# Optimization experiments

Hardware: AMD Instinct MI355X
Metric: run time of the kernel (lower is better)

The kernel has to match this reference:

```python
import jax, jax.numpy as jnp
import numpy as np
import math

BS, SEQ, HID = 1, 2048, 2048
NH, NKV, HD = 32, 8, 64
BASE = 10000.0


def rotate_half(x):
    x1, x2 = x[..., : x.shape[-1] // 2], x[..., x.shape[-1] // 2 :]
    return jnp.concatenate((-x2, x1), axis=-1)


def setup_inputs() -> dict:
    key = jax.random.key(0)
    ks = jax.random.split(key, 6)
    s = 0.02
    return {
        "x": jax.random.normal(ks[0], (BS, SEQ, HID), dtype=jnp.float32),
        "attention_mask": jnp.zeros((BS, SEQ), dtype=jnp.float32),
        "position_ids": jnp.broadcast_to(jnp.arange(SEQ, dtype=jnp.int64 if jax.config.jax_enable_x64 else jnp.int32), (BS, SEQ)),
        "wq": jax.random.normal(ks[1], (HID, NH * HD), dtype=jnp.float32) * s,
        "wk": jax.random.normal(ks[2], (HID, NKV * HD), dtype=jnp.float32) * s,
        "wv": jax.random.normal(ks[3], (HID, NKV * HD), dtype=jnp.float32) * s,
        "wo": jax.random.normal(ks[4], (NH * HD, HID), dtype=jnp.float32) * s,
    }


def reference(x, attention_mask, position_ids, wq, wk, wv, wo):
    bs, seq, _ = x.shape
    groups = NH // NKV

    q = (x @ wq).reshape(bs, seq, NH, HD).transpose(0, 2, 1, 3)   # [b,H,S,D]
    k = (x @ wk).reshape(bs, seq, NKV, HD).transpose(0, 2, 1, 3)  # [b,Hkv,S,D]
    v = (x @ wv).reshape(bs, seq, NKV, HD).transpose(0, 2, 1, 3)

    # rotary embedding
    inv_freq = 1.0 / (BASE ** (jnp.arange(0, HD, 2, dtype=jnp.float32) / HD))  # [D/2]
    freqs = position_ids.astype(jnp.float32)[:, :, None] * inv_freq[None, None, :]  # [b,S,D/2]
    emb = jnp.concatenate((freqs, freqs), axis=-1)               # [b,S,D]
    cos = jnp.cos(emb)[:, None, :, :].astype(x.dtype)            # [b,1,S,D]
    sin = jnp.sin(emb)[:, None, :, :].astype(x.dtype)
    q = q * cos + rotate_half(q) * sin
    k = k * cos + rotate_half(k) * sin

    # repeat_kv (GQA expand)
    k = jnp.repeat(k, groups, axis=1)  # [b,H,S,D]
    v = jnp.repeat(v, groups, axis=1)

    scores = jnp.einsum("bhqd,bhkd->bhqk", q, k) / math.sqrt(HD)
    scores = scores + attention_mask[:, None, None, :]
    attn = jax.nn.softmax(scores.astype(jnp.float32), axis=-1).astype(q.dtype)
    out = jnp.einsum("bhqk,bhkd->bhqd", attn, v)                 # [b,H,S,D]
    out = out.transpose(0, 2, 1, 3).reshape(bs, seq, NH * HD)
    return out @ wo
```

## Files before the change

kernel.cpp:

```cpp
#include <hip/hip_runtime.h>

#define SEQ 2048
#define HID 2048
#define NH  32
#define NKV 8
#define HD  64

typedef _Float16 f16;
typedef __attribute__((ext_vector_type(4))) _Float16 f16x4;
typedef __attribute__((ext_vector_type(8))) _Float16 f16x8;
typedef __attribute__((ext_vector_type(2))) __fp16   h16x2;
typedef __attribute__((ext_vector_type(4))) float    f32x4;

__device__ __forceinline__ f32x4 mfma_16x16x32(f16x8 a, f16x8 b, f32x4 c) {
    return __builtin_amdgcn_mfma_f32_16x16x32_f16(a, b, c, 0, 0, 0);
}

__device__ __forceinline__ void async16(const void* g, void* l) {
    __builtin_amdgcn_global_load_lds(
        (const __attribute__((address_space(1))) void*)g,
        (__attribute__((address_space(3))) void*)l,
        16, 0, 0);
}

__global__ void prep_all(const float* __restrict__ x,
                         const float* __restrict__ wq, const float* __restrict__ wk,
                         const float* __restrict__ wv, const float* __restrict__ wo,
                         f16* __restrict__ xb,
                         f16* __restrict__ Wcat, f16* __restrict__ woT) {
    __shared__ float tile[32][33];
    int z = blockIdx.z;
    int tx = threadIdx.x, ty = threadIdx.y;
    if (z == 4) {
        int idx = (blockIdx.y * 64 + blockIdx.x) * 256 + ty * 32 + tx;
        int i = idx * 4;
        float4 v = *(const float4*)(x + i);
        f16x4 o = { (f16)v.x, (f16)v.y, (f16)v.z, (f16)v.w };
        *(f16x4*)(xb + i) = o;
        return;
    }
    const float* src; f16* dst; int C;
    if      (z == 0) { src = wq; dst = Wcat;                         C = 2048; }
    else if (z == 1) { src = wk; dst = Wcat + (size_t)2048 * 2048;   C = 512;  }
    else if (z == 2) { src = wv; dst = Wcat + (size_t)2560 * 2048;   C = 512;  }
    else             { src = wo; dst = woT;                          C = 2048; }
    int c0 = blockIdx.x * 32, r0 = blockIdx.y * 32;
    if (c0 >= C) return;
#pragma unroll
    for (int i = 0; i < 32; i += 8)
        tile[ty + i][tx] = src[(size_t)(r0 + ty + i) * C + c0 + tx];
    __syncthreads();
#pragma unroll
    for (int i = 0; i < 32; i += 8)
        dst[(size_t)(c0 + ty + i) * 2048 + r0 + tx] = (f16)tile[tx][ty + i];
}

template <int MODE>
__global__ __launch_bounds__(256)
void gemm_bt(const f16* __restrict__ A, const f16* __restrict__ BT,
             float* __restrict__ Cf, f16* __restrict__ Q, f16* __restrict__ Kk,
             f16* __restrict__ VT, const int* __restrict__ pos,
             const float* __restrict__ mask, int N, int K) {
    __shared__ f16 As[2][64 * 64];
    __shared__ f16 Bs[2][128 * 64];
    int t = threadIdx.x;
    int w = t >> 6, lane = t & 63, quad = lane >> 4, l15 = lane & 15;
    int wm = w >> 1, wn = w & 1;
    int m0 = blockIdx.y * 64, n0 = blockIdx.x * 128;
    int sw = l15 & 7;

    int r8 = lane >> 3;
    int cc = (lane & 7) ^ r8;
    const f16* Ag0 = A  + (size_t)(m0 + w * 16 + r8) * K + cc * 8;
    const f16* Ag1 = Ag0 + (size_t)8 * K;
    const f16* Bg  = BT + (size_t)(n0 + w * 32 + r8) * K + cc * 8;

    f32x4 acc[2][4] = {};

    async16(Ag0, &As[0][w * 1024]);
    async16(Ag1, &As[0][w * 1024 + 512]);
#pragma unroll
    for (int g = 0; g < 4; g++)
        async16(Bg + (size_t)(8 * g) * K, &Bs[0][w * 2048 + g * 512]);
    __syncthreads();

    int b = 0;
    for (int kt = 64; kt <= K; kt += 64) {
        if (kt < K) {
            async16(Ag0 + kt, &As[b ^ 1][w * 1024]);
            async16(Ag1 + kt, &As[b ^ 1][w * 1024 + 512]);
#pragma unroll
            for (int g = 0; g < 4; g++)
                async16(Bg + (size_t)(8 * g) * K + kt, &Bs[b ^ 1][w * 2048 + g * 512]);
        }
        f16x8 af[2][2], bf[4][2];
#pragma unroll
        for (int mi = 0; mi < 2; mi++) {
            int row = wm * 32 + mi * 16 + l15;
#pragma unroll
            for (int kh = 0; kh < 2; kh++)
                af[mi][kh] = *(const f16x8*)(&As[b][row * 64 + ((kh * 4 + quad) ^ sw) * 8]);
        }
#pragma unroll
        for (int ni = 0; ni < 4; ni++) {
            int row = wn * 64 + ni * 16 + l15;
#pragma unroll
            for (int kh = 0; kh < 2; kh++)
                bf[ni][kh] = *(const f16x8*)(&Bs[b][row * 64 + ((kh * 4 + quad) ^ sw) * 8]);
        }
#pragma unroll
        for (int mi = 0; mi < 2; mi++)
#pragma unroll
            for (int ni = 0; ni < 4; ni++) {
                acc[mi][ni] = mfma_16x16x32(af[mi][0], bf[ni][0], acc[mi][ni]);
                acc[mi][ni] = mfma_16x16x32(af[mi][1], bf[ni][1], acc[mi][ni]);
            }
        __syncthreads();
        b ^= 1;
    }

    int rb  = m0 + wm * 32 + quad * 4;
    int cbh = n0 + wn * 64;
    if (MODE == 0) {
        if (cbh < (NH + NKV) * HD) {
            bool isQ = cbh < NH * HD;
            f16* dst = isQ ? (Q  + (size_t)(cbh >> 6) * SEQ * HD)
                           : (Kk + (size_t)((cbh - NH * HD) >> 6) * SEQ * HD);
            float scale = isQ ? 0.18033688011112042f : 1.0f;
            float fr[2];
#pragma unroll
            for (int ni = 0; ni < 2; ni++)
                fr[ni] = __builtin_amdgcn_exp2f(
                    (float)(ni * 16 + l15) * -0.41524101186092029f);
#pragma unroll
            for (int mi = 0; mi < 2; mi++)
#pragma unroll
                for (int r = 0; r < 4; r++) {
                    int row = rb + mi * 16 + r;
                    float pv = (float)pos[row];
#pragma unroll
                    for (int ni = 0; ni < 2; ni++) {
                        float sn, cs;
                        __sincosf(pv * fr[ni], &sn, &cs);
                        float x1 = acc[mi][ni][r], x2 = acc[mi][ni + 2][r];
                        int d = ni * 16 + l15;
                        dst[(size_t)row * HD + d]      = (f16)(scale * (x1 * cs - x2 * sn));
                        dst[(size_t)row * HD + d + 32] = (f16)(scale * (x2 * cs + x1 * sn));
                    }
                }
        } else {
            const float LOG2E = 1.4426950408889634f;
#pragma unroll
            for (int mi = 0; mi < 2; mi++) {
                float4 mv = *(const float4*)(mask + rb + mi * 16);
                float em[4];
#pragma unroll
                for (int r = 0; r < 4; r++)
                    em[r] = __builtin_amdgcn_exp2f((&mv.x)[r] * LOG2E);
#pragma unroll
                for (int ni = 0; ni < 4; ni++) {
                    int c2 = cbh - (NH + NKV) * HD + ni * 16 + l15;
                    f16x4 v4;
                    ((h16x2*)&v4)[0] = __builtin_amdgcn_cvt_pkrtz(
                        acc[mi][ni][0] * em[0], acc[mi][ni][1] * em[1]);
                    ((h16x2*)&v4)[1] = __builtin_amdgcn_cvt_pkrtz(
                        acc[mi][ni][2] * em[2], acc[mi][ni][3] * em[3]);
                    *(f16x4*)(VT + (size_t)c2 * SEQ + rb + mi * 16) = v4;
                }
            }
        }
    } else {
#pragma unroll
        for (int mi = 0; mi < 2; mi++)
#pragma unroll
            for (int ni = 0; ni < 4; ni++)
#pragma unroll
                for (int r = 0; r < 4; r++)
                    Cf[(size_t)(rb + mi * 16 + r) * N + cbh + ni * 16 + l15] =
                        acc[mi][ni][r];
    }
}

__global__ __launch_bounds__(512)
void attn_fused(const f16* __restrict__ Qb, const f16* __restrict__ Kb,
                const f16* __restrict__ VTb, const float* __restrict__ mask,
                f16* __restrict__ Opart, float* __restrict__ Lpart) {
    __shared__ f16 Ks[2][64 * 64];
    __shared__ f16 Vs[2][64 * 64];
    __shared__ f16 Em[SEQ / 2];

    int t = threadIdx.x, w = t >> 6, lane = t & 63, quad = lane >> 4, l15 = lane & 15;
    int h = blockIdx.y, kvh = h >> 2, split = blockIdx.z;
    int qbase = blockIdx.x * 256 + w * 32;
    int key0  = split * (SEQ / 2);
    const f16* Qh = Qb  + (size_t)h   * SEQ * HD;
    const f16* Kh = Kb  + (size_t)kvh * SEQ * HD;
    const f16* Vh = VTb + (size_t)kvh * HD * SEQ;
    int sw = l15 & 7;
    const float LOG2E = 1.4426950408889634f;

    if (t < 128) {
        int idx = t * 8;
        float4 ma = *(const float4*)(mask + key0 + idx);
        float4 mb = *(const float4*)(mask + key0 + idx + 4);
        f16x8 e;
        ((h16x2*)&e)[0] = __builtin_amdgcn_cvt_pkrtz(
            __builtin_amdgcn_exp2f(ma.x * LOG2E), __builtin_amdgcn_exp2f(ma.y * LOG2E));
        ((h16x2*)&e)[1] = __builtin_amdgcn_cvt_pkrtz(
            __builtin_amdgcn_exp2f(ma.z * LOG2E), __builtin_amdgcn_exp2f(ma.w * LOG2E));
        ((h16x2*)&e)[2] = __builtin_amdgcn_cvt_pkrtz(
            __builtin_amdgcn_exp2f(mb.x * LOG2E), __builtin_amdgcn_exp2f(mb.y * LOG2E));
        ((h16x2*)&e)[3] = __builtin_amdgcn_cvt_pkrtz(
            __builtin_amdgcn_exp2f(mb.z * LOG2E), __builtin_amdgcn_exp2f(mb.w * LOG2E));
        *(f16x8*)(&Em[idx]) = e;
    }

    int r8 = lane >> 3;
    int cc = (lane & 7) ^ r8;
    bool isK = w < 4;
    int ws = isK ? w : (w - 4);
    const f16* g0;
    long gstep;
    if (isK) {
        int gk = 32 * (ws >> 1) + 4 * (ws & 1) + 8 * (r8 >> 2) + (r8 & 3);
        g0 = Kh + (size_t)(key0 + gk) * HD + cc * 8;
        gstep = (long)16 * HD;
    } else {
        g0 = Vh + (size_t)(ws * 16 + r8) * SEQ + key0 + cc * 8;
        gstep = (long)8 * SEQ;
    }
    const f16* g1 = g0 + gstep;
    long adv = isK ? (long)64 * HD : 64;
    int lr0 = ws * 16 * 64, lr1 = lr0 + 8 * 64;

    {
        f16* dst = isK ? &Ks[0][0] : &Vs[0][0];
        async16(g0, dst + lr0);
        async16(g1, dst + lr1);
    }

    f16x8 bq[2][2];
#pragma unroll
    for (int qg = 0; qg < 2; qg++)
#pragma unroll
        for (int ks = 0; ks < 2; ks++)
            bq[qg][ks] = *(const f16x8*)(Qh + (size_t)(qbase + qg * 16 + l15) * HD
                                            + ks * 32 + quad * 8);

    f32x4 o[4][2] = {};
    f32x4 ol[2]   = {};

    int c0 = (quad ^ sw) * 8, c1 = ((4 | quad) ^ sw) * 8;

    __syncthreads();
    int b = 0;

    for (int ktl = 0; ktl < SEQ / 128; ktl++) {
        if (ktl + 1 < SEQ / 128) {
            g0 += adv; g1 += adv;
            f16* dst = isK ? &Ks[b ^ 1][0] : &Vs[b ^ 1][0];
            async16(g0, dst + lr0);
            async16(g1, dst + lr1);
        }
        const f16* Kb_ = &Ks[b][0];
        const f16* Vb_ = &Vs[b][0];

        f32x4 st[4][2] = {};
#pragma unroll
        for (int ni = 0; ni < 4; ni++) {
            const f16* kr = Kb_ + (ni * 16 + l15) * 64;
            f16x8 ak0 = *(const f16x8*)(kr + c0);
            f16x8 ak1 = *(const f16x8*)(kr + c1);
#pragma unroll
            for (int qg = 0; qg < 2; qg++) {
                st[ni][qg] = mfma_16x16x32(ak0, bq[qg][0], st[ni][qg]);
                st[ni][qg] = mfma_16x16x32(ak1, bq[qg][1], st[ni][qg]);
            }
        }
        f16x8 pb[2][2];
#pragma unroll
        for (int ni = 0; ni < 4; ni++)
#pragma unroll
            for (int qg = 0; qg < 2; qg++) {
                h16x2 lo = __builtin_amdgcn_cvt_pkrtz(
                    __builtin_amdgcn_exp2f(st[ni][qg][0]),
                    __builtin_amdgcn_exp2f(st[ni][qg][1]));
                h16x2 hi = __builtin_amdgcn_cvt_pkrtz(
                    __builtin_amdgcn_exp2f(st[ni][qg][2]),
                    __builtin_amdgcn_exp2f(st[ni][qg][3]));
                ((h16x2*)&pb[qg][ni >> 1])[(ni & 1) * 2]     = lo;
                ((h16x2*)&pb[qg][ni >> 1])[(ni & 1) * 2 + 1] = hi;
            }
        f16x8 em0 = *(const f16x8*)(&Em[ktl * 64 + quad * 8]);
        f16x8 em1 = *(const f16x8*)(&Em[ktl * 64 + 32 + quad * 8]);
#pragma unroll
        for (int qg = 0; qg < 2; qg++) {
            ol[qg] = mfma_16x16x32(em0, pb[qg][0], ol[qg]);
            ol[qg] = mfma_16x16x32(em1, pb[qg][1], ol[qg]);
        }
#pragma unroll
        for (int dt = 0; dt < 4; dt++) {
            const f16* vr = Vb_ + (dt * 16 + l15) * 64;
            f16x8 av0 = *(const f16x8*)(vr + c0);
            f16x8 av1 = *(const f16x8*)(vr + c1);
#pragma unroll
            for (int qg = 0; qg < 2; qg++) {
                o[dt][qg] = mfma_16x16x32(av0, pb[qg][0], o[dt][qg]);
                o[dt][qg] = mfma_16x16x32(av1, pb[qg][1], o[dt][qg]);
            }
        }
        __syncthreads();
        b ^= 1;
    }

    if (quad == 0) {
#pragma unroll
        for (int qg = 0; qg < 2; qg++)
            Lpart[((size_t)split * NH + h) * SEQ + qbase + qg * 16 + l15] =
                ol[qg][0];
    }
    f16* Op = Opart + ((size_t)split * NH + h) * SEQ * HD;
#pragma unroll
    for (int dt = 0; dt < 4; dt++)
#pragma unroll
        for (int qg = 0; qg < 2; qg++) {
            f16x4 v4;
            ((h16x2*)&v4)[0] = __builtin_amdgcn_cvt_pkrtz(o[dt][qg][0], o[dt][qg][1]);
            ((h16x2*)&v4)[1] = __builtin_amdgcn_cvt_pkrtz(o[dt][qg][2], o[dt][qg][3]);
            *(f16x4*)(Op + (size_t)(qbase + qg * 16 + l15) * HD
                         + dt * 16 + quad * 4) = v4;
        }
}

__global__ void attn_combine(const f16* __restrict__ O, const float* __restrict__ L,
                             f16* __restrict__ ctx) {
    int idx = blockIdx.x * 256 + threadIdx.x;
    int c4  = idx & 511;
    int row = idx >> 9;
    int col = c4 * 4;
    int h   = col >> 6;
    float l = L[(size_t)h * SEQ + row] + L[(size_t)(NH + h) * SEQ + row];
    const f16* o0 = O + ((size_t)h * SEQ + row) * HD + (col & 63);
    const f16* o1 = o0 + (size_t)NH * SEQ * HD;
    f16x4 a = *(const f16x4*)o0, b = *(const f16x4*)o1;
    float inv = 1.0f / l;
    f16x4 r;
#pragma unroll
    for (int j = 0; j < 4; j++)
        r[j] = (f16)(((float)a[j] + (float)b[j]) * inv);
    *(f16x4*)(ctx + (size_t)row * (NH * HD) + col) = r;
}

extern "C" void kernel_launch(void* const* d_in, const int* in_sizes, int n_in,
                              void* d_out, int out_size, void* d_ws, size_t ws_size,
                              hipStream_t stream) {
    const float* x    = (const float*)d_in[0];
    const float* mask = (const float*)d_in[1];
    const int*   pos  = (const int*)  d_in[2];
    const float* wq   = (const float*)d_in[3];
    const float* wk   = (const float*)d_in[4];
    const float* wv   = (const float*)d_in[5];
    const float* wo   = (const float*)d_in[6];
    float* out = (float*)d_out;

    char* ws = (char*)d_ws;
    f16*   xb    = (f16*)(ws);
    f16*   Wcat  = (f16*)(ws + ((size_t)8  << 20));
    f16*   woT   = (f16*)(ws + ((size_t)20 << 20));
    f16*   Qb    = (f16*)(ws + ((size_t)28 << 20));
    f16*   Kb    = (f16*)(ws + ((size_t)36 << 20));
    f16*   VTb   = (f16*)(ws + ((size_t)38 << 20));
    f16*   Opart = (f16*)(ws);
    float* Lpart = (float*)(ws + ((size_t)16 << 20));
    f16*   ctx   = (f16*)(ws + ((size_t)28 << 20));

    prep_all<<<dim3(64, 64, 5), dim3(32, 8), 0, stream>>>(
        x, wq, wk, wv, wo, xb, Wcat, woT);

    gemm_bt<0><<<dim3(3072 / 128, 2048 / 64), 256, 0, stream>>>(
        xb, Wcat, nullptr, Qb, Kb, VTb, pos, mask, 3072, 2048);

    attn_fused<<<dim3(SEQ / 256, NH, 2), 512, 0, stream>>>(
        Qb, Kb, VTb, mask, Opart, Lpart);
    attn_combine<<<SEQ * NH * HD / 4 / 256, 256, 0, stream>>>(Opart, Lpart, ctx);

    gemm_bt<1><<<dim3(2048 / 128, 2048 / 64), 256, 0, stream>>>(
        ctx, woT, out, nullptr, nullptr, nullptr, nullptr, nullptr, 2048, 2048);
}
```

Measured before the change: 206.5 us.

## Fuse split-KV combine into output projection GEMM and shrink attention blocks

Removes the separate attn_combine kernel. The output-projection GEMM now reads the two partial attention outputs and row sums directly, normalizing them while staging its A tiles into shared memory. The attention kernel is also cut from 512 to 256 threads per block with 128 queries per block, and every wave now loads both K and V. This saves a launch and a full write and read of the context tensor. In exchange the A operand is loaded synchronously through registers, replacing the async global-to-LDS path, with extra loads and a division per tile.

```diff
diff --git a/kernel.cpp b/kernel.cpp
--- a/kernel.cpp
+++ b/kernel.cpp
@@ -60,7 +60,8 @@
 void gemm_bt(const f16* __restrict__ A, const f16* __restrict__ BT,
              float* __restrict__ Cf, f16* __restrict__ Q, f16* __restrict__ Kk,
              f16* __restrict__ VT, const int* __restrict__ pos,
-             const float* __restrict__ mask, int N, int K) {
+             const float* __restrict__ mask, const float* __restrict__ Lp,
+             int N, int K) {
     __shared__ f16 As[2][64 * 64];
     __shared__ f16 Bs[2][128 * 64];
     int t = threadIdx.x;
@@ -75,10 +76,41 @@
     const f16* Ag1 = Ag0 + (size_t)8 * K;
     const f16* Bg  = BT + (size_t)(n0 + w * 32 + r8) * K + cc * 8;
 
+    int arow0 = m0 + w * 16 + r8;
+    int arow1 = arow0 + 8;
+
     f32x4 acc[2][4] = {};
 
-    async16(Ag0, &As[0][w * 1024]);
-    async16(Ag1, &As[0][w * 1024 + 512]);
+    auto stageA1 = [&](int koff, int buf) {
+        int hh = koff >> 6;
+        const f16* b0 = A + (size_t)hh * SEQ * HD + cc * 8;
+        const f16* b1 = b0 + (size_t)NH * SEQ * HD;
+        float li0 = 1.0f / (Lp[hh * SEQ + arow0] + Lp[(NH + hh) * SEQ + arow0]);
+        float li1 = 1.0f / (Lp[hh * SEQ + arow1] + Lp[(NH + hh) * SEQ + arow1]);
+        f16x8 a00 = *(const f16x8*)(b0 + (size_t)arow0 * HD);
+        f16x8 a01 = *(const f16x8*)(b1 + (size_t)arow0 * HD);
+        f16x8 a10 = *(const f16x8*)(b0 + (size_t)arow1 * HD);
+        f16x8 a11 = *(const f16x8*)(b1 + (size_t)arow1 * HD);
+        f16x8 r0v, r1v;
+#pragma unroll
+        for (int j = 0; j < 4; j++) {
+            ((h16x2*)&r0v)[j] = __builtin_amdgcn_cvt_pkrtz(
+                ((float)a00[2 * j]     + (float)a01[2 * j])     * li0,
+                ((float)a00[2 * j + 1] + (float)a01[2 * j + 1]) * li0);
+            ((h16x2*)&r1v)[j] = __builtin_amdgcn_cvt_pkrtz(
+                ((float)a10[2 * j]     + (float)a11[2 * j])     * li1,
+                ((float)a10[2 * j + 1] + (float)a11[2 * j + 1]) * li1);
+        }
+        *(f16x8*)(&As[buf][w * 1024 + lane * 8])       = r0v;
+        *(f16x8*)(&As[buf][w * 1024 + 512 + lane * 8]) = r1v;
+    };
+
+    if (MODE == 0) {
+        async16(Ag0, &As[0][w * 1024]);
+        async16(Ag1, &As[0][w * 1024 + 512]);
+    } else {
+        stageA1(0, 0);
+    }
 #pragma unroll
     for (int g = 0; g < 4; g++)
         async16(Bg + (size_t)(8 * g) * K, &Bs[0][w * 2048 + g * 512]);
@@ -87,8 +119,12 @@
     int b = 0;
     for (int kt = 64; kt <= K; kt += 64) {
         if (kt < K) {
-            async16(Ag0 + kt, &As[b ^ 1][w * 1024]);
-            async16(Ag1 + kt, &As[b ^ 1][w * 1024 + 512]);
+            if (MODE == 0) {
+                async16(Ag0 + kt, &As[b ^ 1][w * 1024]);
+                async16(Ag1 + kt, &As[b ^ 1][w * 1024 + 512]);
+            } else {
+                stageA1(kt, b ^ 1);
+            }
 #pragma unroll
             for (int g = 0; g < 4; g++)
                 async16(Bg + (size_t)(8 * g) * K + kt, &Bs[b ^ 1][w * 2048 + g * 512]);
@@ -181,7 +217,7 @@
     }
 }
 
-__global__ __launch_bounds__(512)
+__global__ __launch_bounds__(256)
 void attn_fused(const f16* __restrict__ Qb, const f16* __restrict__ Kb,
                 const f16* __restrict__ VTb, const float* __restrict__ mask,
                 f16* __restrict__ Opart, float* __restrict__ Lpart) {
@@ -191,7 +227,7 @@
 
     int t = threadIdx.x, w = t >> 6, lane = t & 63, quad = lane >> 4, l15 = lane & 15;
     int h = blockIdx.y, kvh = h >> 2, split = blockIdx.z;
-    int qbase = blockIdx.x * 256 + w * 32;
+    int qbase = blockIdx.x * 128 + w * 32;
     int key0  = split * (SEQ / 2);
     const f16* Qh = Qb  + (size_t)h   * SEQ * HD;
     const f16* Kh = Kb  + (size_t)kvh * SEQ * HD;
@@ -217,27 +253,17 @@
 
     int r8 = lane >> 3;
     int cc = (lane & 7) ^ r8;
-    bool isK = w < 4;
-    int ws = isK ? w : (w - 4);
-    const f16* g0;
-    long gstep;
-    if (isK) {
-        int gk = 32 * (ws >> 1) + 4 * (ws & 1) + 8 * (r8 >> 2) + (r8 & 3);
-        g0 = Kh + (size_t)(key0 + gk) * HD + cc * 8;
-        gstep = (long)16 * HD;
-    } else {
-        g0 = Vh + (size_t)(ws * 16 + r8) * SEQ + key0 + cc * 8;
-        gstep = (long)8 * SEQ;
-    }
-    const f16* g1 = g0 + gstep;
-    long adv = isK ? (long)64 * HD : 64;
-    int lr0 = ws * 16 * 64, lr1 = lr0 + 8 * 64;
-
-    {
-        f16* dst = isK ? &Ks[0][0] : &Vs[0][0];
-        async16(g0, dst + lr0);
-        async16(g1, dst + lr1);
-    }
+    int gk = 32 * (w >> 1) + 4 * (w & 1) + 8 * (r8 >> 2) + (r8 & 3);
+    const f16* kg0 = Kh + (size_t)(key0 + gk) * HD + cc * 8;
+    const f16* kg1 = kg0 + (size_t)16 * HD;
+    const f16* vg0 = Vh + (size_t)(w * 16 + r8) * SEQ + key0 + cc * 8;
+    const f16* vg1 = vg0 + 8 * SEQ;
+    int lr0 = (w * 16) * 64, lr1 = (w * 16 + 8) * 64;
+
+    async16(kg0, &Ks[0][lr0]);
+    async16(kg1, &Ks[0][lr1]);
+    async16(vg0, &Vs[0][lr0]);
+    async16(vg1, &Vs[0][lr1]);
 
     f16x8 bq[2][2];
 #pragma unroll
@@ -257,10 +283,11 @@
 
     for (int ktl = 0; ktl < SEQ / 128; ktl++) {
         if (ktl + 1 < SEQ / 128) {
-            g0 += adv; g1 += adv;
-            f16* dst = isK ? &Ks[b ^ 1][0] : &Vs[b ^ 1][0];
-            async16(g0, dst + lr0);
-            async16(g1, dst + lr1);
+            kg0 += 64 * HD; kg1 += 64 * HD; vg0 += 64; vg1 += 64;
+            async16(kg0, &Ks[b ^ 1][lr0]);
+            async16(kg1, &Ks[b ^ 1][lr1]);
+            async16(vg0, &Vs[b ^ 1][lr0]);
+            async16(vg1, &Vs[b ^ 1][lr1]);
         }
         const f16* Kb_ = &Ks[b][0];
         const f16* Vb_ = &Vs[b][0];
@@ -330,25 +357,6 @@
             *(f16x4*)(Op + (size_t)(qbase + qg * 16 + l15) * HD
                          + dt * 16 + quad * 4) = v4;
         }
-}
-
-__global__ void attn_combine(const f16* __restrict__ O, const float* __restrict__ L,
-                             f16* __restrict__ ctx) {
-    int idx = blockIdx.x * 256 + threadIdx.x;
-    int c4  = idx & 511;
-    int row = idx >> 9;
-    int col = c4 * 4;
-    int h   = col >> 6;
-    float l = L[(size_t)h * SEQ + row] + L[(size_t)(NH + h) * SEQ + row];
-    const f16* o0 = O + ((size_t)h * SEQ + row) * HD + (col & 63);
-    const f16* o1 = o0 + (size_t)NH * SEQ * HD;
-    f16x4 a = *(const f16x4*)o0, b = *(const f16x4*)o1;
-    float inv = 1.0f / l;
-    f16x4 r;
-#pragma unroll
-    for (int j = 0; j < 4; j++)
-        r[j] = (f16)(((float)a[j] + (float)b[j]) * inv);
-    *(f16x4*)(ctx + (size_t)row * (NH * HD) + col) = r;
 }
 
 extern "C" void kernel_launch(void* const* d_in, const int* in_sizes, int n_in,
@@ -372,18 +380,17 @@
     f16*   VTb   = (f16*)(ws + ((size_t)38 << 20));
     f16*   Opart = (f16*)(ws);
     float* Lpart = (float*)(ws + ((size_t)16 << 20));
-    f16*   ctx   = (f16*)(ws + ((size_t)28 << 20));
 
     prep_all<<<dim3(64, 64, 5), dim3(32, 8), 0, stream>>>(
         x, wq, wk, wv, wo, xb, Wcat, woT);
 
     gemm_bt<0><<<dim3(3072 / 128, 2048 / 64), 256, 0, stream>>>(
-        xb, Wcat, nullptr, Qb, Kb, VTb, pos, mask, 3072, 2048);
-
-    attn_fused<<<dim3(SEQ / 256, NH, 2), 512, 0, stream>>>(
+        xb, Wcat, nullptr, Qb, Kb, VTb, pos, mask, nullptr, 3072, 2048);
+
+    attn_fused<<<dim3(SEQ / 128, NH, 2), 256, 0, stream>>>(
         Qb, Kb, VTb, mask, Opart, Lpart);
-    attn_combine<<<SEQ * NH * HD / 4 / 256, 256, 0, stream>>>(Opart, Lpart, ctx);
 
     gemm_bt<1><<<dim3(2048 / 128, 2048 / 64), 256, 0, stream>>>(
-        ctx, woT, out, nullptr, nullptr, nullptr, nullptr, nullptr, 2048, 2048);
-}
+        Opart, woT, out, nullptr, nullptr, nullptr, nullptr, nullptr, Lpart,
+        2048, 2048);
+}
```

Result: slower. 233.8 us (+13.2%).
